# Kernel tuning notes

Hardware: AMD Instinct MI355X
Metric: run time of the kernel (lower is better)

## Reference

```python
import jax, jax.numpy as jnp
import numpy as np

N, DIM = 4096, 1024

def setup_inputs() -> dict:
    key = jax.random.key(0)
    ks = jax.random.split(key, 5)
    scale = 1.0 / np.sqrt(DIM)
    return {
        "x": jax.random.normal(ks[0], (N, DIM), dtype=jnp.float32),
        "Wq": jax.random.normal(ks[1], (DIM, DIM), dtype=jnp.float32) * scale,
        "bq": jax.random.normal(ks[2], (DIM,), dtype=jnp.float32) * 0.01,
        "Wk": jax.random.normal(ks[3], (DIM, DIM), dtype=jnp.float32) * scale,
        "bk": jax.random.normal(ks[4], (DIM,), dtype=jnp.float32) * 0.01,
    }

def reference(x, Wq, bq, Wk, bk):
    # torch nn.Linear: y = x @ W.T + b
    q = x @ Wq.T + bq            # [N, D]
    k = x @ Wk.T + bk            # [N, D]
    scores = q @ k.T             # [N, N] (no 1/sqrt(d) scaling, as in source)
    attn = jax.nn.softmax(scores, axis=-1)
    return attn @ x              # weighted pooling over raw x (no value proj)
```

## Files before the change

kernel.cpp:

```cpp
#include <hip/hip_runtime.h>
#include <hip/hip_bf16.h>
#include <hip/hip_fp16.h>
#include <stdint.h>


using half8   = __attribute__((ext_vector_type(8))) _Float16;
using float4v = __attribute__((ext_vector_type(4))) float;
using int4v   = __attribute__((ext_vector_type(4))) int;

#define QS        (6.0f / 32768.0f)
#define INV_S     (32768.0f / 6.0f)
#define INV_S256  (128.0f / 6.0f)
#define C_HH      (65536.0f * QS * QS)
#define C_X       (256.0f * QS * QS)

#define SX        (6.0f / 32768.0f)
#define SW        (0.25f / 32768.0f)
#define P_HH      (65536.0f * SX * SW)
#define P_X       (256.0f * SX * SW)

#define GLOAD_LDS16(gptr, ldsptr)                                              \
  __builtin_amdgcn_global_load_lds(                                            \
      (__attribute__((address_space(1))) void*)(uintptr_t)(gptr),              \
      (__attribute__((address_space(3))) void*)(unsigned)(uintptr_t)(ldsptr),  \
      16, 0, 0)

__device__ __forceinline__ void barrier_raw() {
  asm volatile("" ::: "memory");
  __builtin_amdgcn_s_barrier();
  asm volatile("" ::: "memory");
}

__global__ __launch_bounds__(256, 2) void gemm_s_stats(
    const int8_t* __restrict__ Ahi, const int8_t* __restrict__ Alo,
    const int8_t* __restrict__ Bhi, const int8_t* __restrict__ Blo,
    _Float16* __restrict__ E, float2* __restrict__ stats)
{
  __shared__ __align__(16) int8_t sAh[2][128 * 64];
  __shared__ __align__(16) int8_t sAl[2][128 * 64];
  __shared__ __align__(16) int8_t sBh[2][128 * 64];
  __shared__ __align__(16) int8_t sBl[2][128 * 64];

  const int tid  = threadIdx.x;
  const int wave = tid >> 6;
  const int lane = tid & 63;
  const int quad = lane >> 4;
  const int t16  = lane & 15;
  const int wm   = wave & 1;
  const int wn   = wave >> 1;
  const int row0 = blockIdx.y * 128;
  const int col0 = blockIdx.x * 128;

  const int seg  = lane & 3;
  const int rsub = lane >> 2;
  const int segS = seg ^ (rsub & 3);
  const int rch  = (quad ^ (t16 & 3)) * 16;

  int4v hh[4][4], cc[4][4];
#pragma unroll
  for (int i = 0; i < 4; ++i)
#pragma unroll
    for (int j = 0; j < 4; ++j) {
      hh[i][j] = (int4v){0, 0, 0, 0};
      cc[i][j] = (int4v){0, 0, 0, 0};
    }

  auto stage_k = [&](int ks, int b) {
    const int k0 = ks * 64;
#pragma unroll
    for (int r = 0; r < 2; ++r) {
      const int trow = r * 64 + wave * 16;
      const size_t goffA = (size_t)(row0 + trow + rsub) * 2048 + k0 + segS * 16;
      const size_t goffB = (size_t)(col0 + trow + rsub) * 2048 + k0 + segS * 16;
      GLOAD_LDS16(Ahi + goffA, &sAh[b][trow * 64]);
      GLOAD_LDS16(Alo + goffA, &sAl[b][trow * 64]);
      GLOAD_LDS16(Bhi + goffB, &sBh[b][trow * 64]);
      GLOAD_LDS16(Blo + goffB, &sBl[b][trow * 64]);
    }
  };

  stage_k(0, 0);
  int buf = 0;
  for (int ks = 0; ks < 16; ++ks) {
    if (ks < 15) {
      stage_k(ks + 1, buf ^ 1);
      asm volatile("s_waitcnt vmcnt(8)" ::: "memory");
    } else {
      asm volatile("s_waitcnt vmcnt(0)" ::: "memory");
    }
    barrier_raw();

    int4v ah[4], al[4], bh[4], bl[4];
#pragma unroll
    for (int i = 0; i < 4; ++i) {
      const int ao = (wm * 64 + i * 16 + t16) * 64 + rch;
      ah[i] = *(const int4v*)&sAh[buf][ao];
      al[i] = *(const int4v*)&sAl[buf][ao];
    }
#pragma unroll
    for (int j = 0; j < 4; ++j) {
      const int bo = (wn * 64 + j * 16 + t16) * 64 + rch;
      bh[j] = *(const int4v*)&sBh[buf][bo];
      bl[j] = *(const int4v*)&sBl[buf][bo];
    }

#pragma unroll
    for (int i = 0; i < 4; ++i)
#pragma unroll
      for (int j = 0; j < 4; ++j) {
        hh[i][j] = __builtin_amdgcn_mfma_i32_16x16x64_i8(ah[i], bh[j], hh[i][j], 0, 0, 0);
        cc[i][j] = __builtin_amdgcn_mfma_i32_16x16x64_i8(ah[i], bl[j], cc[i][j], 0, 0, 0);
        cc[i][j] = __builtin_amdgcn_mfma_i32_16x16x64_i8(al[i], bh[j], cc[i][j], 0, 0, 0);
      }
    barrier_raw();
    buf ^= 1;
  }

  float* red = (float*)sAh;

  float vv[4][4][4];
  float rmax[4][4];
#pragma unroll
  for (int i = 0; i < 4; ++i)
#pragma unroll
    for (int r = 0; r < 4; ++r) {
      float mx = -3.0e38f;
#pragma unroll
      for (int j = 0; j < 4; ++j) {
        float v = C_HH * (float)hh[i][j][r] + C_X * (float)cc[i][j][r];
        vv[i][j][r] = v;
        mx = fmaxf(mx, v);
      }
      mx = fmaxf(mx, __shfl_xor(mx, 1));
      mx = fmaxf(mx, __shfl_xor(mx, 2));
      mx = fmaxf(mx, __shfl_xor(mx, 4));
      mx = fmaxf(mx, __shfl_xor(mx, 8));
      rmax[i][r] = mx;
    }
  if (t16 == 0) {
#pragma unroll
    for (int i = 0; i < 4; ++i)
#pragma unroll
      for (int r = 0; r < 4; ++r)
        red[wn * 128 + wm * 64 + i * 16 + quad * 4 + r] = rmax[i][r];
  }
  __syncthreads();

  float mrow[4][4];
#pragma unroll
  for (int i = 0; i < 4; ++i)
#pragma unroll
    for (int r = 0; r < 4; ++r) {
      const int row = wm * 64 + i * 16 + quad * 4 + r;
      mrow[i][r] = fmaxf(red[row], red[128 + row]);
    }

  float rsum[4][4];
#pragma unroll
  for (int i = 0; i < 4; ++i)
#pragma unroll
    for (int r = 0; r < 4; ++r) {
      float s = 0.f;
#pragma unroll
      for (int j = 0; j < 4; ++j) {
        float e = __expf(vv[i][j][r] - mrow[i][r]);
        vv[i][j][r] = e;
        s += e;
      }
      s += __shfl_xor(s, 1);
      s += __shfl_xor(s, 2);
      s += __shfl_xor(s, 4);
      s += __shfl_xor(s, 8);
      rsum[i][r] = s;
    }
  if (t16 == 0) {
#pragma unroll
    for (int i = 0; i < 4; ++i)
#pragma unroll
      for (int r = 0; r < 4; ++r)
        red[256 + wn * 128 + wm * 64 + i * 16 + quad * 4 + r] = rsum[i][r];
  }
  __syncthreads();

#pragma unroll
  for (int i = 0; i < 4; ++i) {
#pragma unroll
    for (int j = 0; j < 4; ++j) {
#pragma unroll
      for (int r = 0; r < 4; ++r) {
        const int crow = row0 + wm * 64 + i * 16 + quad * 4 + r;
        const int ccol = col0 + wn * 64 + j * 16 + t16;
        E[(size_t)crow * 4096 + ccol] = (_Float16)vv[i][j][r];
      }
    }
  }
  if (wn == 0 && t16 == 0) {
#pragma unroll
    for (int i = 0; i < 4; ++i)
#pragma unroll
      for (int r = 0; r < 4; ++r) {
        const int row = wm * 64 + i * 16 + quad * 4 + r;
        const float l = red[256 + row] + red[256 + 128 + row];
        stats[(size_t)(row0 + row) * 32 + blockIdx.x] =
            make_float2(mrow[i][r], l);
      }
  }
}

__global__ __launch_bounds__(256, 2) void gemm_proj_i8(
    const int8_t* __restrict__ Ahi, const int8_t* __restrict__ Alo,
    const int8_t* __restrict__ Bhi, const int8_t* __restrict__ Blo,
    const float* __restrict__ biasQ, const float* __restrict__ biasK,
    int8_t* __restrict__ Ch, int8_t* __restrict__ Cl)
{
  __shared__ __align__(16) int8_t sAh[2][128 * 64];
  __shared__ __align__(16) int8_t sAl[2][128 * 64];
  __shared__ __align__(16) int8_t sBh[2][128 * 64];
  __shared__ __align__(16) int8_t sBl[2][128 * 64];

  const int tid  = threadIdx.x;
  const int wave = tid >> 6;
  const int lane = tid & 63;
  const int quad = lane >> 4;
  const int t16  = lane & 15;
  const int wm   = wave & 1;
  const int wn   = wave >> 1;
  const int row0 = blockIdx.y * 128;
  const int col0 = blockIdx.x * 128;

  const int seg  = lane & 3;
  const int rsub = lane >> 2;
  const int segS = seg ^ (rsub & 3);
  const int rch  = (quad ^ (t16 & 3)) * 16;

  int4v hh[4][4], cc[4][4];
#pragma unroll
  for (int i = 0; i < 4; ++i)
#pragma unroll
    for (int j = 0; j < 4; ++j) {
      hh[i][j] = (int4v){0, 0, 0, 0};
      cc[i][j] = (int4v){0, 0, 0, 0};
    }

  auto stage_k = [&](int ks, int b) {
    const int k0 = ks * 64;
#pragma unroll
    for (int r = 0; r < 2; ++r) {
      const int trow = r * 64 + wave * 16;
      const size_t goffA = (size_t)(row0 + trow + rsub) * 1024 + k0 + segS * 16;
      const size_t goffB = (size_t)(col0 + trow + rsub) * 1024 + k0 + segS * 16;
      GLOAD_LDS16(Ahi + goffA, &sAh[b][trow * 64]);
      GLOAD_LDS16(Alo + goffA, &sAl[b][trow * 64]);
      GLOAD_LDS16(Bhi + goffB, &sBh[b][trow * 64]);
      GLOAD_LDS16(Blo + goffB, &sBl[b][trow * 64]);
    }
  };

  stage_k(0, 0);
  int buf = 0;
  for (int ks = 0; ks < 16; ++ks) {
    if (ks < 15) {
      stage_k(ks + 1, buf ^ 1);
      asm volatile("s_waitcnt vmcnt(8)" ::: "memory");
    } else {
      asm volatile("s_waitcnt vmcnt(0)" ::: "memory");
    }
    barrier_raw();

    int4v ah[4], al[4], bh[4], bl[4];
#pragma unroll
    for (int i = 0; i < 4; ++i) {
      const int ao = (wm * 64 + i * 16 + t16) * 64 + rch;
      ah[i] = *(const int4v*)&sAh[buf][ao];
      al[i] = *(const int4v*)&sAl[buf][ao];
    }
#pragma unroll
    for (int j = 0; j < 4; ++j) {
      const int bo = (wn * 64 + j * 16 + t16) * 64 + rch;
      bh[j] = *(const int4v*)&sBh[buf][bo];
      bl[j] = *(const int4v*)&sBl[buf][bo];
    }

#pragma unroll
    for (int i = 0; i < 4; ++i)
#pragma unroll
      for (int j = 0; j < 4; ++j) {
        hh[i][j] = __builtin_amdgcn_mfma_i32_16x16x64_i8(ah[i], bh[j], hh[i][j], 0, 0, 0);
        cc[i][j] = __builtin_amdgcn_mfma_i32_16x16x64_i8(ah[i], bl[j], cc[i][j], 0, 0, 0);
        cc[i][j] = __builtin_amdgcn_mfma_i32_16x16x64_i8(al[i], bh[j], cc[i][j], 0, 0, 0);
      }
    barrier_raw();
    buf ^= 1;
  }

#pragma unroll
  for (int i = 0; i < 4; ++i) {
#pragma unroll
    for (int j = 0; j < 4; ++j) {
      const int ccol = col0 + wn * 64 + j * 16 + t16;
      const float* bp = (ccol < 1024) ? biasQ : (biasK - 1024);
#pragma unroll
      for (int r = 0; r < 4; ++r) {
        const int crow = row0 + wm * 64 + i * 16 + quad * 4 + r;
        float v = P_HH * (float)hh[i][j][r] + P_X * (float)cc[i][j][r] + bp[ccol];
        int hi = (int)lrintf(v * INV_S256);
        hi = hi > 127 ? 127 : (hi < -127 ? -127 : hi);
        int lo = (int)lrintf(v * INV_S - 256.0f * (float)hi);
        lo = lo > 127 ? 127 : (lo < -127 ? -127 : lo);
        Ch[(size_t)crow * 2048 + ccol] = (int8_t)hi;
        Cl[(size_t)crow * 2048 + ccol] = (int8_t)lo;
      }
    }
  }
}

__global__ __launch_bounds__(512) void gemm_av(
    const uint16_t* __restrict__ E, const uint16_t* __restrict__ B,
    const float2* __restrict__ stats, float* __restrict__ out)
{
  __shared__ __align__(16) uint16_t stage[2][16384];
  __shared__ float betaS[128 * 33];

  const int L      = blockIdx.x;
  const int xcd    = L & 7;
  const int rest   = L >> 3;
  const int colb   = rest & 7;
  const int bandHi = rest >> 3;
  const int band   = xcd + 8 * bandHi;
  const int row0   = band * 128;
  const int col0   = colb * 128;

  const int tid  = threadIdx.x;
  const int wave = tid >> 6;
  const int z    = wave >> 2;
  const int gw   = wave & 3;
  const int lane = tid & 63;
  const int quad = lane >> 4;
  const int t16  = lane & 15;
  const int wm   = gw & 1;
  const int wn   = gw >> 1;
  const int seg  = lane & 3;
  const int rsub = lane >> 2;
  const int segS = seg ^ (rsub & 3);
  const int rch8 = (quad ^ (t16 & 3)) * 8;

  if (tid < 128) {
    const int row = row0 + tid;
    float2 st[32];
    float m = -3.0e38f;
#pragma unroll
    for (int t = 0; t < 32; ++t) {
      st[t] = stats[(size_t)row * 32 + t];
      m = fmaxf(m, st[t].x);
    }
    float l = 0.f;
#pragma unroll
    for (int t = 0; t < 32; ++t) l += st[t].y * __expf(st[t].x - m);
    const float inv = 1.0f / l;
#pragma unroll
    for (int t = 0; t < 32; ++t)
      betaS[tid * 33 + t] = __expf(st[t].x - m) * inv;
  }
  __syncthreads();

  float4v acc[4][4];
#pragma unroll
  for (int i = 0; i < 4; ++i)
#pragma unroll
    for (int j = 0; j < 4; ++j)
      acc[i][j] = (float4v){0.f, 0.f, 0.f, 0.f};

  auto stage_s = [&](int s, int b) {
    const int k0 = (z * 16 + (s >> 2)) * 128 + (s & 3) * 32;
    uint16_t* sA = &stage[b][z * 8192];
    uint16_t* sB = &stage[b][z * 8192 + 4096];
#pragma unroll
    for (int r = 0; r < 2; ++r) {
      const int trow = r * 64 + gw * 16;
      const size_t goffA = (size_t)(row0 + trow + rsub) * 4096 + k0 + segS * 8;
      const size_t goffB = (size_t)(col0 + trow + rsub) * 4096 + k0 + segS * 8;
      GLOAD_LDS16(E + goffA, &sA[trow * 32]);
      GLOAD_LDS16(B + goffB, &sB[trow * 32]);
    }
  };

  stage_s(0, 0);
  int buf = 0;
  for (int s = 0; s < 64; ++s) {
    if (s < 63) {
      stage_s(s + 1, buf ^ 1);
      asm volatile("s_waitcnt vmcnt(4)" ::: "memory");
    } else {
      asm volatile("s_waitcnt vmcnt(0)" ::: "memory");
    }
    barrier_raw();

    const int t = z * 16 + (s >> 2);
    _Float16 bb[4];
#pragma unroll
    for (int i = 0; i < 4; ++i)
      bb[i] = (_Float16)betaS[(wm * 64 + i * 16 + t16) * 33 + t];

    const uint16_t* sA = &stage[buf][z * 8192];
    const uint16_t* sB = &stage[buf][z * 8192 + 4096];

    half8 af[4], bf[4];
#pragma unroll
    for (int i = 0; i < 4; ++i) {
      af[i] = *(const half8*)&sA[(wm * 64 + i * 16 + t16) * 32 + rch8];
      half8 bs;
#pragma unroll
      for (int c = 0; c < 8; ++c) bs[c] = bb[i];
      af[i] = af[i] * bs;
    }
#pragma unroll
    for (int j = 0; j < 4; ++j)
      bf[j] = *(const half8*)&sB[(wn * 64 + j * 16 + t16) * 32 + rch8];

#pragma unroll
    for (int i = 0; i < 4; ++i)
#pragma unroll
      for (int j = 0; j < 4; ++j)
        acc[i][j] = __builtin_amdgcn_mfma_f32_16x16x32_f16(af[i], bf[j], acc[i][j], 0, 0, 0);

    barrier_raw();
    buf ^= 1;
  }

  float* xfer = (float*)stage;
#pragma unroll
  for (int h = 0; h < 2; ++h) {
    if (z == 1) {
#pragma unroll
      for (int i = 2 * h; i < 2 * h + 2; ++i)
#pragma unroll
        for (int j = 0; j < 4; ++j)
#pragma unroll
          for (int r = 0; r < 4; ++r) {
            const int e = (i - 2 * h) * 16 + j * 4 + r;
            xfer[e * 256 + gw * 64 + lane] = acc[i][j][r];
          }
    }
    __syncthreads();
    if (z == 0) {
#pragma unroll
      for (int i = 2 * h; i < 2 * h + 2; ++i)
#pragma unroll
        for (int j = 0; j < 4; ++j)
#pragma unroll
          for (int r = 0; r < 4; ++r) {
            const int e = (i - 2 * h) * 16 + j * 4 + r;
            acc[i][j][r] += xfer[e * 256 + gw * 64 + lane];
          }
    }
    __syncthreads();
  }

  if (z == 0) {
#pragma unroll
    for (int i = 0; i < 4; ++i) {
#pragma unroll
      for (int j = 0; j < 4; ++j) {
        const int ccol = col0 + wn * 64 + j * 16 + t16;
#pragma unroll
        for (int r = 0; r < 4; ++r) {
          const int crow = row0 + wm * 64 + i * 16 + quad * 4 + r;
          out[(size_t)crow * 1024 + ccol] = acc[i][j][r];
        }
      }
    }
  }
}

__global__ __launch_bounds__(256) void quantT(
    const float* __restrict__ x, const float* __restrict__ Wq,
    const float* __restrict__ Wk,
    int8_t* __restrict__ xhi, int8_t* __restrict__ xlo,
    int8_t* __restrict__ whi, int8_t* __restrict__ wlo,
    uint16_t* __restrict__ xT)
{
  if (blockIdx.x < 6144) {
    int i = blockIdx.x * 256 + threadIdx.x;
    const float* src; int8_t* dh; int8_t* dl; int idx; float s256, s;
    if (i < 1048576)      { src = x;  idx = i;           dh = xhi; dl = xlo;
                            s256 = INV_S256; s = INV_S; }
    else if (i < 1310720) { src = Wq; idx = i - 1048576; dh = whi; dl = wlo;
                            s256 = 512.0f; s = 131072.0f; }
    else                  { src = Wk; idx = i - 1310720; dh = whi + 1048576;
                            dl = wlo + 1048576; s256 = 512.0f; s = 131072.0f; }
    float4 v = ((const float4*)src)[idx];
    float vv[4] = {v.x, v.y, v.z, v.w};
    int hp = 0, lp = 0;
#pragma unroll
    for (int c = 0; c < 4; ++c) {
      int h = (int)lrintf(vv[c] * s256);
      h = h > 127 ? 127 : (h < -127 ? -127 : h);
      int l = (int)lrintf(vv[c] * s - 256.0f * (float)h);
      l = l > 127 ? 127 : (l < -127 ? -127 : l);
      hp |= (h & 0xff) << (8 * c);
      lp |= (l & 0xff) << (8 * c);
    }
    ((int*)dh)[idx] = hp;
    ((int*)dl)[idx] = lp;
  } else {
    __shared__ float tile[32][33];
    const int tb = blockIdx.x - 6144;
    const int bx = tb & 31;
    const int by = tb >> 5;
    const int tx = threadIdx.x & 31;
    const int ty = threadIdx.x >> 5;
#pragma unroll
    for (int p = 0; p < 4; ++p) {
      const int row = by * 32 + ty + p * 8;
      tile[ty + p * 8][tx] = x[(size_t)row * 1024 + bx * 32 + tx];
    }
    __syncthreads();
#pragma unroll
    for (int p = 0; p < 4; ++p) {
      const int oc = ty + p * 8;
      __half hv = __float2half_rn(tile[tx][oc]);
      xT[(size_t)(bx * 32 + oc) * 4096 + by * 32 + tx] = *(uint16_t*)&hv;
    }
  }
}

extern "C" void kernel_launch(void* const* d_in, const int* in_sizes, int n_in,
                              void* d_out, int out_size, void* d_ws, size_t ws_size,
                              hipStream_t stream) {
  const int N = 4096, D = 1024;
  const float* x  = (const float*)d_in[0];
  const float* Wq = (const float*)d_in[1];
  const float* bq = (const float*)d_in[2];
  const float* Wk = (const float*)d_in[3];
  const float* bk = (const float*)d_in[4];
  float* out = (float*)d_out;

  char* w = (char*)d_ws;
  const size_t MiB = 1024 * 1024;
  int8_t*    xq_hi  = (int8_t*)   (w + 0  * MiB);
  int8_t*    xq_lo  = (int8_t*)   (w + 4  * MiB);
  int8_t*    Wqk_hi = (int8_t*)   (w + 8  * MiB);
  int8_t*    Wqk_lo = (int8_t*)   (w + 10 * MiB);
  int8_t*    qk_hi  = (int8_t*)   (w + 12 * MiB);
  int8_t*    qk_lo  = (int8_t*)   (w + 20 * MiB);
  _Float16*  E      = (_Float16*) (w + 36 * MiB);
  float2*    stats  = (float2*)   (w + 68 * MiB);
  uint16_t*  xTh    = (uint16_t*) (w + 72 * MiB);

  quantT<<<10240, 256, 0, stream>>>(x, Wq, Wk, xq_hi, xq_lo, Wqk_hi, Wqk_lo,
                                    xTh);

  gemm_proj_i8<<<dim3(2048 / 128, N / 128), 256, 0, stream>>>(
      xq_hi, xq_lo, Wqk_hi, Wqk_lo, bq, bk, qk_hi, qk_lo);

  gemm_s_stats<<<dim3(N / 128, N / 128), 256, 0, stream>>>(
      qk_hi, qk_lo, qk_hi + 1024, qk_lo + 1024, E, stats);

  gemm_av<<<256, 512, 0, stream>>>((const uint16_t*)E, xTh, stats, out);

  (void)in_sizes; (void)n_in; (void)out_size; (void)ws_size;
}
```

Before: 221.8 us.

## Restructure GEMM pipelines: single barrier per step, wider AV K-tile, setprio around MFMAs

The two int8 split-precision GEMM kernels now precompute global and LDS offsets, drop the XOR swizzle, and move to one barrier per k-step, waiting on outstanding loads after the MFMA block instead of before it. The AV GEMM doubles its K-tile to 64 halves per stage, halving iterations and barriers. It uses a rotated-chunk swizzle and issues the first stage before the softmax-stat prologue to overlap it. s_setprio brackets the MFMA loops. Removing the swizzle in the int8 kernels risks LDS bank conflicts, and the larger AV stage doubles LDS use, which may reduce occupancy.

```diff
diff --git a/kernel.cpp b/kernel.cpp
--- a/kernel.cpp
+++ b/kernel.cpp
@@ -53,8 +53,13 @@
 
   const int seg  = lane & 3;
   const int rsub = lane >> 2;
-  const int segS = seg ^ (rsub & 3);
-  const int rch  = (quad ^ (t16 & 3)) * 16;
+
+  const int offA0 = (row0 + wave * 16 + rsub) * 2048 + seg * 16;
+  const int offA1 = offA0 + 64 * 2048;
+  const int offB0 = (col0 + wave * 16 + rsub) * 2048 + seg * 16;
+  const int offB1 = offB0 + 64 * 2048;
+  const int ldsT0 = (wave * 16) * 64;
+  const int ldsT1 = (64 + wave * 16) * 64;
 
   int4v hh[4][4], cc[4][4];
 #pragma unroll
@@ -67,43 +72,39 @@
 
   auto stage_k = [&](int ks, int b) {
     const int k0 = ks * 64;
-#pragma unroll
-    for (int r = 0; r < 2; ++r) {
-      const int trow = r * 64 + wave * 16;
-      const size_t goffA = (size_t)(row0 + trow + rsub) * 2048 + k0 + segS * 16;
-      const size_t goffB = (size_t)(col0 + trow + rsub) * 2048 + k0 + segS * 16;
-      GLOAD_LDS16(Ahi + goffA, &sAh[b][trow * 64]);
-      GLOAD_LDS16(Alo + goffA, &sAl[b][trow * 64]);
-      GLOAD_LDS16(Bhi + goffB, &sBh[b][trow * 64]);
-      GLOAD_LDS16(Blo + goffB, &sBl[b][trow * 64]);
-    }
+    GLOAD_LDS16(Ahi + offA0 + k0, &sAh[b][ldsT0]);
+    GLOAD_LDS16(Ahi + offA1 + k0, &sAh[b][ldsT1]);
+    GLOAD_LDS16(Alo + offA0 + k0, &sAl[b][ldsT0]);
+    GLOAD_LDS16(Alo + offA1 + k0, &sAl[b][ldsT1]);
+    GLOAD_LDS16(Bhi + offB0 + k0, &sBh[b][ldsT0]);
+    GLOAD_LDS16(Bhi + offB1 + k0, &sBh[b][ldsT1]);
+    GLOAD_LDS16(Blo + offB0 + k0, &sBl[b][ldsT0]);
+    GLOAD_LDS16(Blo + offB1 + k0, &sBl[b][ldsT1]);
   };
 
   stage_k(0, 0);
+  asm volatile("s_waitcnt vmcnt(0)" ::: "memory");
+  barrier_raw();
+
   int buf = 0;
   for (int ks = 0; ks < 16; ++ks) {
-    if (ks < 15) {
-      stage_k(ks + 1, buf ^ 1);
-      asm volatile("s_waitcnt vmcnt(8)" ::: "memory");
-    } else {
-      asm volatile("s_waitcnt vmcnt(0)" ::: "memory");
-    }
-    barrier_raw();
+    if (ks < 15) stage_k(ks + 1, buf ^ 1);
 
     int4v ah[4], al[4], bh[4], bl[4];
 #pragma unroll
     for (int i = 0; i < 4; ++i) {
-      const int ao = (wm * 64 + i * 16 + t16) * 64 + rch;
+      const int ao = (wm * 64 + i * 16 + t16) * 64 + quad * 16;
       ah[i] = *(const int4v*)&sAh[buf][ao];
       al[i] = *(const int4v*)&sAl[buf][ao];
     }
 #pragma unroll
     for (int j = 0; j < 4; ++j) {
-      const int bo = (wn * 64 + j * 16 + t16) * 64 + rch;
+      const int bo = (wn * 64 + j * 16 + t16) * 64 + quad * 16;
       bh[j] = *(const int4v*)&sBh[buf][bo];
       bl[j] = *(const int4v*)&sBl[buf][bo];
     }
 
+    __builtin_amdgcn_s_setprio(1);
 #pragma unroll
     for (int i = 0; i < 4; ++i)
 #pragma unroll
@@ -112,6 +113,9 @@
         cc[i][j] = __builtin_amdgcn_mfma_i32_16x16x64_i8(ah[i], bl[j], cc[i][j], 0, 0, 0);
         cc[i][j] = __builtin_amdgcn_mfma_i32_16x16x64_i8(al[i], bh[j], cc[i][j], 0, 0, 0);
       }
+    __builtin_amdgcn_s_setprio(0);
+
+    if (ks < 15) asm volatile("s_waitcnt vmcnt(0)" ::: "memory");
     barrier_raw();
     buf ^= 1;
   }
@@ -230,8 +234,13 @@
 
   const int seg  = lane & 3;
   const int rsub = lane >> 2;
-  const int segS = seg ^ (rsub & 3);
-  const int rch  = (quad ^ (t16 & 3)) * 16;
+
+  const int offA0 = (row0 + wave * 16 + rsub) * 1024 + seg * 16;
+  const int offA1 = offA0 + 64 * 1024;
+  const int offB0 = (col0 + wave * 16 + rsub) * 1024 + seg * 16;
+  const int offB1 = offB0 + 64 * 1024;
+  const int ldsT0 = (wave * 16) * 64;
+  const int ldsT1 = (64 + wave * 16) * 64;
 
   int4v hh[4][4], cc[4][4];
 #pragma unroll
@@ -244,43 +253,39 @@
 
   auto stage_k = [&](int ks, int b) {
     const int k0 = ks * 64;
-#pragma unroll
-    for (int r = 0; r < 2; ++r) {
-      const int trow = r * 64 + wave * 16;
-      const size_t goffA = (size_t)(row0 + trow + rsub) * 1024 + k0 + segS * 16;
-      const size_t goffB = (size_t)(col0 + trow + rsub) * 1024 + k0 + segS * 16;
-      GLOAD_LDS16(Ahi + goffA, &sAh[b][trow * 64]);
-      GLOAD_LDS16(Alo + goffA, &sAl[b][trow * 64]);
-      GLOAD_LDS16(Bhi + goffB, &sBh[b][trow * 64]);
-      GLOAD_LDS16(Blo + goffB, &sBl[b][trow * 64]);
-    }
+    GLOAD_LDS16(Ahi + offA0 + k0, &sAh[b][ldsT0]);
+    GLOAD_LDS16(Ahi + offA1 + k0, &sAh[b][ldsT1]);
+    GLOAD_LDS16(Alo + offA0 + k0, &sAl[b][ldsT0]);
+    GLOAD_LDS16(Alo + offA1 + k0, &sAl[b][ldsT1]);
+    GLOAD_LDS16(Bhi + offB0 + k0, &sBh[b][ldsT0]);
+    GLOAD_LDS16(Bhi + offB1 + k0, &sBh[b][ldsT1]);
+    GLOAD_LDS16(Blo + offB0 + k0, &sBl[b][ldsT0]);
+    GLOAD_LDS16(Blo + offB1 + k0, &sBl[b][ldsT1]);
   };
 
   stage_k(0, 0);
+  asm volatile("s_waitcnt vmcnt(0)" ::: "memory");
+  barrier_raw();
+
   int buf = 0;
   for (int ks = 0; ks < 16; ++ks) {
-    if (ks < 15) {
-      stage_k(ks + 1, buf ^ 1);
-      asm volatile("s_waitcnt vmcnt(8)" ::: "memory");
-    } else {
-      asm volatile("s_waitcnt vmcnt(0)" ::: "memory");
-    }
-    barrier_raw();
+    if (ks < 15) stage_k(ks + 1, buf ^ 1);
 
     int4v ah[4], al[4], bh[4], bl[4];
 #pragma unroll
     for (int i = 0; i < 4; ++i) {
-      const int ao = (wm * 64 + i * 16 + t16) * 64 + rch;
+      const int ao = (wm * 64 + i * 16 + t16) * 64 + quad * 16;
       ah[i] = *(const int4v*)&sAh[buf][ao];
       al[i] = *(const int4v*)&sAl[buf][ao];
     }
 #pragma unroll
     for (int j = 0; j < 4; ++j) {
-      const int bo = (wn * 64 + j * 16 + t16) * 64 + rch;
+      const int bo = (wn * 64 + j * 16 + t16) * 64 + quad * 16;
       bh[j] = *(const int4v*)&sBh[buf][bo];
       bl[j] = *(const int4v*)&sBl[buf][bo];
     }
 
+    __builtin_amdgcn_s_setprio(1);
 #pragma unroll
     for (int i = 0; i < 4; ++i)
 #pragma unroll
@@ -289,6 +294,9 @@
         cc[i][j] = __builtin_amdgcn_mfma_i32_16x16x64_i8(ah[i], bl[j], cc[i][j], 0, 0, 0);
         cc[i][j] = __builtin_amdgcn_mfma_i32_16x16x64_i8(al[i], bh[j], cc[i][j], 0, 0, 0);
       }
+    __builtin_amdgcn_s_setprio(0);
+
+    if (ks < 15) asm volatile("s_waitcnt vmcnt(0)" ::: "memory");
     barrier_raw();
     buf ^= 1;
   }
@@ -318,7 +326,7 @@
     const uint16_t* __restrict__ E, const uint16_t* __restrict__ B,
     const float2* __restrict__ stats, float* __restrict__ out)
 {
-  __shared__ __align__(16) uint16_t stage[2][16384];
+  __shared__ __align__(16) uint16_t stg[2][2][16384];
   __shared__ float betaS[128 * 33];
 
   const int L      = blockIdx.x;
@@ -339,10 +347,30 @@
   const int t16  = lane & 15;
   const int wm   = gw & 1;
   const int wn   = gw >> 1;
-  const int seg  = lane & 3;
-  const int rsub = lane >> 2;
-  const int segS = seg ^ (rsub & 3);
-  const int rch8 = (quad ^ (t16 & 3)) * 8;
+
+  const int c8   = lane & 7;
+  const int r8   = lane >> 3;
+  const int srcC = (c8 - r8) & 7;
+
+  int offA[4], offB[4];
+#pragma unroll
+  for (int r = 0; r < 4; ++r) {
+    offA[r] = (row0 + r * 32 + gw * 8 + r8) * 4096 + srcC * 8;
+    offB[r] = (col0 + r * 32 + gw * 8 + r8) * 4096 + srcC * 8;
+  }
+
+  auto stage_s = [&](int s, int b) {
+    const int k0h = (z * 16 + (s >> 1)) * 128 + (s & 1) * 64;
+    uint16_t* sA = &stg[b][z][0];
+    uint16_t* sB = &stg[b][z][8192];
+#pragma unroll
+    for (int r = 0; r < 4; ++r) {
+      GLOAD_LDS16(E + offA[r] + k0h, &sA[(r * 32 + gw * 8) * 64]);
+      GLOAD_LDS16(B + offB[r] + k0h, &sB[(r * 32 + gw * 8) * 64]);
+    }
+  };
+
+  stage_s(0, 0);
 
   if (tid < 128) {
     const int row = row0 + tid;
@@ -361,6 +389,7 @@
     for (int t = 0; t < 32; ++t)
       betaS[tid * 33 + t] = __expf(st[t].x - m) * inv;
   }
+  asm volatile("s_waitcnt vmcnt(0)" ::: "memory");
   __syncthreads();
 
   float4v acc[4][4];
@@ -370,64 +399,56 @@
     for (int j = 0; j < 4; ++j)
       acc[i][j] = (float4v){0.f, 0.f, 0.f, 0.f};
 
-  auto stage_s = [&](int s, int b) {
-    const int k0 = (z * 16 + (s >> 2)) * 128 + (s & 3) * 32;
-    uint16_t* sA = &stage[b][z * 8192];
-    uint16_t* sB = &stage[b][z * 8192 + 4096];
-#pragma unroll
-    for (int r = 0; r < 2; ++r) {
-      const int trow = r * 64 + gw * 16;
-      const size_t goffA = (size_t)(row0 + trow + rsub) * 4096 + k0 + segS * 8;
-      const size_t goffB = (size_t)(col0 + trow + rsub) * 4096 + k0 + segS * 8;
-      GLOAD_LDS16(E + goffA, &sA[trow * 32]);
-      GLOAD_LDS16(B + goffB, &sB[trow * 32]);
-    }
-  };
-
-  stage_s(0, 0);
   int buf = 0;
-  for (int s = 0; s < 64; ++s) {
-    if (s < 63) {
-      stage_s(s + 1, buf ^ 1);
-      asm volatile("s_waitcnt vmcnt(4)" ::: "memory");
-    } else {
-      asm volatile("s_waitcnt vmcnt(0)" ::: "memory");
-    }
-    barrier_raw();
-
-    const int t = z * 16 + (s >> 2);
+  for (int s = 0; s < 32; ++s) {
+    if (s < 31) stage_s(s + 1, buf ^ 1);
+
+    const int t = z * 16 + (s >> 1);
     _Float16 bb[4];
 #pragma unroll
     for (int i = 0; i < 4; ++i)
       bb[i] = (_Float16)betaS[(wm * 64 + i * 16 + t16) * 33 + t];
 
-    const uint16_t* sA = &stage[buf][z * 8192];
-    const uint16_t* sB = &stage[buf][z * 8192 + 4096];
-
-    half8 af[4], bf[4];
-#pragma unroll
-    for (int i = 0; i < 4; ++i) {
-      af[i] = *(const half8*)&sA[(wm * 64 + i * 16 + t16) * 32 + rch8];
-      half8 bs;
-#pragma unroll
-      for (int c = 0; c < 8; ++c) bs[c] = bb[i];
-      af[i] = af[i] * bs;
-    }
-#pragma unroll
-    for (int j = 0; j < 4; ++j)
-      bf[j] = *(const half8*)&sB[(wn * 64 + j * 16 + t16) * 32 + rch8];
-
-#pragma unroll
-    for (int i = 0; i < 4; ++i)
-#pragma unroll
-      for (int j = 0; j < 4; ++j)
-        acc[i][j] = __builtin_amdgcn_mfma_f32_16x16x32_f16(af[i], bf[j], acc[i][j], 0, 0, 0);
-
+    const uint16_t* sA = &stg[buf][z][0];
+    const uint16_t* sB = &stg[buf][z][8192];
+
+    half8 af[2][4], bf[2][4];
+#pragma unroll
+    for (int ks = 0; ks < 2; ++ks) {
+#pragma unroll
+      for (int i = 0; i < 4; ++i) {
+        const int row = wm * 64 + i * 16 + t16;
+        const int ch  = (ks * 4 + quad + (t16 & 7)) & 7;
+        af[ks][i] = *(const half8*)&sA[row * 64 + ch * 8];
+        half8 bs;
+#pragma unroll
+        for (int c = 0; c < 8; ++c) bs[c] = bb[i];
+        af[ks][i] = af[ks][i] * bs;
+      }
+#pragma unroll
+      for (int j = 0; j < 4; ++j) {
+        const int row = wn * 64 + j * 16 + t16;
+        const int ch  = (ks * 4 + quad + (t16 & 7)) & 7;
+        bf[ks][j] = *(const half8*)&sB[row * 64 + ch * 8];
+      }
+    }
+
+    __builtin_amdgcn_s_setprio(1);
+#pragma unroll
+    for (int ks = 0; ks < 2; ++ks)
+#pragma unroll
+      for (int i = 0; i < 4; ++i)
+#pragma unroll
+        for (int j = 0; j < 4; ++j)
+          acc[i][j] = __builtin_amdgcn_mfma_f32_16x16x32_f16(af[ks][i], bf[ks][j], acc[i][j], 0, 0, 0);
+    __builtin_amdgcn_s_setprio(0);
+
+    if (s < 31) asm volatile("s_waitcnt vmcnt(0)" ::: "memory");
     barrier_raw();
     buf ^= 1;
   }
 
-  float* xfer = (float*)stage;
+  float* xfer = (float*)stg;
 #pragma unroll
   for (int h = 0; h < 2; ++h) {
     if (z == 1) {
```

New measurement: 218.9 us. No clear change (-1.3%).
